# Optimization experiments

Hardware: AMD Instinct MI355X
Metric: run time of the kernel (lower is better)

## Reference

```python
import jax, jax.numpy as jnp
jax.config.update("jax_enable_x64", True)  # faithful to .double() matmul in original
import numpy as np

QMAX = 127.0  # int8 target: get_quant_min_max(torch.int8)[1]


def setup_inputs() -> dict:
    key = jax.random.key(0)
    k1, k2, k3, k4 = jax.random.split(key, 4)
    x = jax.random.normal(k1, (32768, 1024), dtype=jnp.float32)          # [tokens, cin]
    weight = jax.random.normal(k2, (1024, 1024), dtype=jnp.float32) * 0.02  # [cout, cin]
    bias = jax.random.normal(k3, (1024,), dtype=jnp.float32)             # [cout]
    # per-tensor activation scale from the (fake) observer; keep strictly positive
    act_scale = jax.random.uniform(k4, (1,), dtype=jnp.float32) * 0.05 + 0.01
    return {"x": x, "weight": weight, "bias": bias, "act_scale": act_scale}


def reference(x, weight, bias, act_scale):
    s = act_scale[0]  # per-tensor act scale; scale_input = 1/s
    # --- set_quantized_mode math ---
    w_scaled = weight * s                                        # fold act scale into weight (per-cin, per-tensor here)
    weight_scale = jnp.max(jnp.abs(w_scaled), axis=1) / QMAX     # [cout] per-output-channel scale
    qw = jnp.round(w_scaled / weight_scale[:, None])             # int8-valued weights (stored as float)
    # --- quantized forward ---
    xq = jnp.round(jnp.clip(x / s, -QMAX, QMAX))                 # fake-quant activations
    acc = jnp.matmul(xq.astype(jnp.float64), qw.astype(jnp.float64).T)  # double-precision GEMM
    y = acc.astype(jnp.float32) * weight_scale[None, :] + bias   # dequant rescale + bias
    return y
```

## Files before the change

### kernel.cpp

```cpp
#include <hip/hip_runtime.h>

typedef int i32x4 __attribute__((ext_vector_type(4)));

#define QMAXF 127.0f

__global__ __launch_bounds__(256) void quant_w_kernel(
    const float* __restrict__ w, const float* __restrict__ act_scale,
    signed char* __restrict__ qw, float* __restrict__ wscale)
{
    const int row = blockIdx.x;
    const int t   = threadIdx.x;
    const float s = act_scale[0];

    float4 v = *reinterpret_cast<const float4*>(w + (size_t)row * 1024 + t * 4);
    float a0 = v.x * s, a1 = v.y * s, a2 = v.z * s, a3 = v.w * s;
    float m = fmaxf(fmaxf(fabsf(a0), fabsf(a1)), fmaxf(fabsf(a2), fabsf(a3)));

    #pragma unroll
    for (int i = 1; i < 64; i <<= 1)
        m = fmaxf(m, __shfl_xor(m, i));

    __shared__ float wmax[4];
    if ((t & 63) == 0) wmax[t >> 6] = m;
    __syncthreads();
    m = fmaxf(fmaxf(wmax[0], wmax[1]), fmaxf(wmax[2], wmax[3]));

    const float wsc = m / QMAXF;

    int q0 = (int)rintf(a0 / wsc);
    int q1 = (int)rintf(a1 / wsc);
    int q2 = (int)rintf(a2 / wsc);
    int q3 = (int)rintf(a3 / wsc);
    int packed = (q0 & 255) | ((q1 & 255) << 8) | ((q2 & 255) << 16) | ((q3 & 255) << 24);
    reinterpret_cast<int*>(qw)[row * 256 + t] = packed;

    if (t == 0) wscale[row] = wsc;
}

__global__ __launch_bounds__(256) void quant_x_kernel(
    const float* __restrict__ x, const float* __restrict__ act_scale,
    signed char* __restrict__ xq)
{
    const float s = act_scale[0];
    const size_t i = ((size_t)blockIdx.x * 256 + threadIdx.x) * 4;
    float4 v = *reinterpret_cast<const float4*>(x + i);
    int q0 = (int)rintf(fminf(fmaxf(v.x / s, -QMAXF), QMAXF));
    int q1 = (int)rintf(fminf(fmaxf(v.y / s, -QMAXF), QMAXF));
    int q2 = (int)rintf(fminf(fmaxf(v.z / s, -QMAXF), QMAXF));
    int q3 = (int)rintf(fminf(fmaxf(v.w / s, -QMAXF), QMAXF));
    int packed = (q0 & 255) | ((q1 & 255) << 8) | ((q2 & 255) << 16) | ((q3 & 255) << 24);
    reinterpret_cast<int*>(xq)[i >> 2] = packed;
}

#define BM 256
#define BN 256
#define BKB 128
#define NTILES 8

#define BAR()   __builtin_amdgcn_s_barrier()
#define LGKM0() asm volatile("s_waitcnt lgkmcnt(0)" ::: "memory")

__global__ __launch_bounds__(512, 2) void gemm_i8_kernel(
    const signed char* __restrict__ xq, const signed char* __restrict__ qw,
    const float* __restrict__ wscale, const float* __restrict__ bias,
    float* __restrict__ out, int M)
{
    const int K = 1024, N = 1024;
    __shared__ __align__(16) signed char lds[2 * 2 * 2 * 16384];

    const int t    = threadIdx.x;
    const int lane = t & 63;
    const int w    = t >> 6;
    const int wr   = w >> 2;
    const int wc   = w & 3;
    const int lrow = lane & 15;
    const int ks   = lane >> 4;
    const int r8   = lane >> 3;
    const int sl   = lane & 7;

    const int nwg = gridDim.x;
    const int cpx = nwg >> 3;
    const int bid = blockIdx.x;
    const int swz = (bid & 7) * cpx + (bid >> 3);
    const int m0 = (swz >> 2) * BM;
    const int n0 = (swz & 3) * BN;

    i32x4 acc[8][4] = {};
    i32x4 Ar[4][2];
    i32x4 Br[2][2][2];

    auto STAGE = [&](int kt, int ab, int h) {
        const signed char* g = ab ? qw : xq;
        const int grow0 = (ab ? n0 : m0) + h * 128;
        signed char* lb = lds + (((kt & 1) * 2 + ab) * 2 + h) * 16384;
        #pragma unroll
        for (int j = 0; j < 2; ++j) {
            const int row = (j * 8 + w) * 8 + r8;
            const signed char* src =
                g + (size_t)(grow0 + row) * K + kt * BKB + ((sl ^ r8) << 4);
            __builtin_amdgcn_global_load_lds(
                (const __attribute__((address_space(1))) void*)src,
                (__attribute__((address_space(3))) void*)(lb + ((j * 8 + w) * 64 + lane) * 16),
                16, 0, 0);
        }
    };

    auto LDA = [&](int buf, int mh, i32x4 A[4][2]) {
        const signed char* base = lds + ((buf * 2 + 0) * 2 + wr) * 16384;
        #pragma unroll
        for (int mf = 0; mf < 4; ++mf) {
            const int row = mh * 64 + mf * 16 + lrow;
            #pragma unroll
            for (int kk = 0; kk < 2; ++kk) {
                const int slot = (kk * 4 + ks) ^ (lrow & 7);
                A[mf][kk] = *reinterpret_cast<const i32x4*>(base + row * 128 + slot * 16);
            }
        }
    };
    auto LDB = [&](int buf, int nh, i32x4 B[2][2]) {
        const signed char* base = lds + ((buf * 2 + 1) * 2 + (wc >> 1)) * 16384;
        #pragma unroll
        for (int nf = 0; nf < 2; ++nf) {
            const int row = (wc & 1) * 64 + nh * 32 + nf * 16 + lrow;
            #pragma unroll
            for (int kk = 0; kk < 2; ++kk) {
                const int slot = (kk * 4 + ks) ^ (lrow & 7);
                B[nf][kk] = *reinterpret_cast<const i32x4*>(base + row * 128 + slot * 16);
            }
        }
    };
    auto MM = [&](int mh, int nh, i32x4 A[4][2], i32x4 B[2][2]) {
        __builtin_amdgcn_s_setprio(1);
        #pragma unroll
        for (int mf = 0; mf < 4; ++mf)
            #pragma unroll
            for (int nf = 0; nf < 2; ++nf)
                #pragma unroll
                for (int kk = 0; kk < 2; ++kk)
                    acc[mh * 4 + mf][nh * 2 + nf] = __builtin_amdgcn_mfma_i32_16x16x64_i8(
                        A[mf][kk], B[nf][kk], acc[mh * 4 + mf][nh * 2 + nf], 0, 0, 0);
        __builtin_amdgcn_s_setprio(0);
    };

    STAGE(0, 1, 0); STAGE(0, 1, 1); STAGE(0, 0, 0); STAGE(0, 0, 1);
    STAGE(1, 1, 0); STAGE(1, 1, 1);
    asm volatile("s_waitcnt vmcnt(4)" ::: "memory");
    BAR();

    #pragma unroll
    for (int it = 0; it < NTILES / 2; ++it) {
        const int T = 2 * it;
        LDA(0, 0, Ar); LDB(0, 0, Br[0]);
        STAGE(T + 1, 0, 0);
        BAR(); LGKM0();
        MM(0, 0, Ar, Br[0]);
        BAR();
        LDB(0, 1, Br[1]);
        STAGE(T + 1, 0, 1);
        BAR(); LGKM0();
        MM(0, 1, Ar, Br[1]);
        BAR();
        LDA(0, 1, Ar);
        if (T + 2 < NTILES) STAGE(T + 2, 1, 0);
        BAR(); LGKM0();
        MM(1, 0, Ar, Br[0]);
        BAR();
        if (T + 2 < NTILES) STAGE(T + 2, 1, 1);
        MM(1, 1, Ar, Br[1]);
        if (T + 2 < NTILES) { asm volatile("s_waitcnt vmcnt(4)" ::: "memory"); }
        else                { asm volatile("s_waitcnt vmcnt(0)" ::: "memory"); }
        BAR();
        LDA(1, 0, Ar); LDB(1, 0, Br[0]);
        if (T + 2 < NTILES) STAGE(T + 2, 0, 0);
        BAR(); LGKM0();
        MM(0, 0, Ar, Br[0]);
        BAR();
        LDB(1, 1, Br[1]);
        if (T + 2 < NTILES) STAGE(T + 2, 0, 1);
        BAR(); LGKM0();
        MM(0, 1, Ar, Br[1]);
        BAR();
        LDA(1, 1, Ar);
        if (T + 3 < NTILES) STAGE(T + 3, 1, 0);
        BAR(); LGKM0();
        MM(1, 0, Ar, Br[0]);
        BAR();
        if (T + 3 < NTILES) STAGE(T + 3, 1, 1);
        MM(1, 1, Ar, Br[1]);
        if (T + 3 < NTILES) { asm volatile("s_waitcnt vmcnt(4)" ::: "memory"); }
        BAR();
    }

    float wsv[4], bv[4];
    int   gnc[4];
    #pragma unroll
    for (int nf = 0; nf < 4; ++nf) {
        const int gn = n0 + wc * 64 + nf * 16 + lrow;
        gnc[nf] = gn;
        wsv[nf] = wscale[gn];
        bv[nf]  = bias[gn];
    }
    #pragma unroll
    for (int mf = 0; mf < 8; ++mf) {
        #pragma unroll
        for (int r = 0; r < 4; ++r) {
            const int gm = m0 + wr * 128 + mf * 16 + ks * 4 + r;
            float* orow = out + (size_t)gm * N;
            #pragma unroll
            for (int nf = 0; nf < 4; ++nf)
                orow[gnc[nf]] = (float)acc[mf][nf][r] * wsv[nf] + bv[nf];
        }
    }
}

extern "C" void kernel_launch(void* const* d_in, const int* in_sizes, int n_in,
                              void* d_out, int out_size, void* d_ws, size_t ws_size,
                              hipStream_t stream)
{
    const float* x         = (const float*)d_in[0];
    const float* weight    = (const float*)d_in[1];
    const float* bias      = (const float*)d_in[2];
    const float* act_scale = (const float*)d_in[3];
    float* out             = (float*)d_out;

    const int K = 1024;
    const int N = 1024;
    const int M = in_sizes[0] / K;

    char* wsb = (char*)d_ws;
    signed char* qw  = (signed char*)wsb;
    float*       wsc = (float*)(wsb + (size_t)N * K);
    signed char* xq  = (signed char*)(wsb + (size_t)N * K + 4096);

    quant_w_kernel<<<N, 256, 0, stream>>>(weight, act_scale, qw, wsc);
    quant_x_kernel<<<(int)(((size_t)M * K) / 1024), 256, 0, stream>>>(x, act_scale, xq);

    const int grid = (M / BM) * (N / BN);
    gemm_i8_kernel<<<grid, 512, 0, stream>>>(xq, qw, wsc, bias, out, M);
}
```

Measured before the change: 86.35 us.

## Fuse activation quantization into int8 GEMM A-tile staging

Removes the separate activation-quantization kernel and its int8 intermediate buffer. The GEMM now loads fp32 x tiles into registers, quantizes them (multiplying by a reciprocal scale), and writes swizzled int8 into LDS. Only the weight tiles still go through direct global-to-LDS loads. The goal is to save one kernel launch plus the write and re-read of the quantized activations. In exchange, x is read as fp32 by each of the four column-tile blocks, which relies on L2 reuse. It also adds register pressure from the staged float4 buffers and drops the explicit vmcnt waits in favour of compiler-inserted waits.

Measured after the change: 216.3 us. +150.4%, slower.

```diff
diff --git a/kernel.cpp b/kernel.cpp
--- a/kernel.cpp
+++ b/kernel.cpp
@@ -3,6 +3,8 @@
 typedef int i32x4 __attribute__((ext_vector_type(4)));
 
 #define QMAXF 127.0f
+#define LGKM0() asm volatile("s_waitcnt lgkmcnt(0)" ::: "memory")
+#define BAR()   __builtin_amdgcn_s_barrier()
 
 __global__ __launch_bounds__(256) void quant_w_kernel(
     const float* __restrict__ w, const float* __restrict__ act_scale,
@@ -37,36 +39,16 @@
     if (t == 0) wscale[row] = wsc;
 }
 
-__global__ __launch_bounds__(256) void quant_x_kernel(
-    const float* __restrict__ x, const float* __restrict__ act_scale,
-    signed char* __restrict__ xq)
-{
-    const float s = act_scale[0];
-    const size_t i = ((size_t)blockIdx.x * 256 + threadIdx.x) * 4;
-    float4 v = *reinterpret_cast<const float4*>(x + i);
-    int q0 = (int)rintf(fminf(fmaxf(v.x / s, -QMAXF), QMAXF));
-    int q1 = (int)rintf(fminf(fmaxf(v.y / s, -QMAXF), QMAXF));
-    int q2 = (int)rintf(fminf(fmaxf(v.z / s, -QMAXF), QMAXF));
-    int q3 = (int)rintf(fminf(fmaxf(v.w / s, -QMAXF), QMAXF));
-    int packed = (q0 & 255) | ((q1 & 255) << 8) | ((q2 & 255) << 16) | ((q3 & 255) << 24);
-    reinterpret_cast<int*>(xq)[i >> 2] = packed;
-}
-
-#define BM 256
-#define BN 256
-#define BKB 128
 #define NTILES 8
 
-#define BAR()   __builtin_amdgcn_s_barrier()
-#define LGKM0() asm volatile("s_waitcnt lgkmcnt(0)" ::: "memory")
-
-__global__ __launch_bounds__(512, 2) void gemm_i8_kernel(
-    const signed char* __restrict__ xq, const signed char* __restrict__ qw,
-    const float* __restrict__ wscale, const float* __restrict__ bias,
-    float* __restrict__ out, int M)
+__global__ __launch_bounds__(512, 2) void gemm_fused_kernel(
+    const float* __restrict__ x, const signed char* __restrict__ qw,
+    const float* __restrict__ act_scale, const float* __restrict__ wscale,
+    const float* __restrict__ bias, float* __restrict__ out, int M)
 {
     const int K = 1024, N = 1024;
-    __shared__ __align__(16) signed char lds[2 * 2 * 2 * 16384];
+    __shared__ __align__(16) signed char As[4][16384];
+    __shared__ __align__(16) signed char Bs[4][16384];
 
     const int t    = threadIdx.x;
     const int lane = t & 63;
@@ -77,48 +59,72 @@
     const int ks   = lane >> 4;
     const int r8   = lane >> 3;
     const int sl   = lane & 7;
+    const int ar   = t >> 2;
+    const int ac2  = t & 3;
 
     const int nwg = gridDim.x;
     const int cpx = nwg >> 3;
     const int bid = blockIdx.x;
     const int swz = (bid & 7) * cpx + (bid >> 3);
-    const int m0 = (swz >> 2) * BM;
-    const int n0 = (swz & 3) * BN;
+    const int m0 = (swz >> 2) * 256;
+    const int n0 = (swz & 3) * 256;
+
+    const float rinv = 1.0f / act_scale[0];
 
     i32x4 acc[8][4] = {};
     i32x4 Ar[4][2];
     i32x4 Br[2][2][2];
-
-    auto STAGE = [&](int kt, int ab, int h) {
-        const signed char* g = ab ? qw : xq;
-        const int grow0 = (ab ? n0 : m0) + h * 128;
-        signed char* lb = lds + (((kt & 1) * 2 + ab) * 2 + h) * 16384;
+    float4 X0[8], X1[8];
+
+    auto STAGE_B = [&](int kt, int h) {
+        signed char* lb = &Bs[(kt & 1) * 2 + h][0];
         #pragma unroll
         for (int j = 0; j < 2; ++j) {
-            const int row = (j * 8 + w) * 8 + r8;
+            const int rowh = (j * 8 + w) * 8 + r8;
             const signed char* src =
-                g + (size_t)(grow0 + row) * K + kt * BKB + ((sl ^ r8) << 4);
+                qw + (size_t)(n0 + h * 128 + rowh) * K + kt * 128 + ((sl ^ r8) << 4);
             __builtin_amdgcn_global_load_lds(
                 (const __attribute__((address_space(1))) void*)src,
                 (__attribute__((address_space(3))) void*)(lb + ((j * 8 + w) * 64 + lane) * 16),
                 16, 0, 0);
         }
     };
-
-    auto LDA = [&](int buf, int mh, i32x4 A[4][2]) {
-        const signed char* base = lds + ((buf * 2 + 0) * 2 + wr) * 16384;
+    auto XLD = [&](int kt, int h, float4 (&X)[8]) {
+        const float* p = x + (size_t)(m0 + h * 128 + ar) * K + kt * 128 + ac2 * 32;
+        #pragma unroll
+        for (int j = 0; j < 8; ++j) X[j] = *reinterpret_cast<const float4*>(p + j * 4);
+    };
+    auto AQW = [&](int kt, int h, const float4 (&X)[8]) {
+        int pk[8];
+        #pragma unroll
+        for (int c = 0; c < 8; ++c) {
+            int q0 = (int)rintf(fminf(fmaxf(X[c].x * rinv, -QMAXF), QMAXF));
+            int q1 = (int)rintf(fminf(fmaxf(X[c].y * rinv, -QMAXF), QMAXF));
+            int q2 = (int)rintf(fminf(fmaxf(X[c].z * rinv, -QMAXF), QMAXF));
+            int q3 = (int)rintf(fminf(fmaxf(X[c].w * rinv, -QMAXF), QMAXF));
+            pk[c] = (q0 & 255) | ((q1 & 255) << 8) | ((q2 & 255) << 16) | ((q3 & 255) << 24);
+        }
+        signed char* base = &As[(kt & 1) * 2 + h][0];
+        const int g0 = 2 * ac2, g1 = 2 * ac2 + 1;
+        *reinterpret_cast<i32x4*>(base + ar * 128 + ((g0 ^ (ar & 7)) << 4)) =
+            i32x4{pk[0], pk[1], pk[2], pk[3]};
+        *reinterpret_cast<i32x4*>(base + ar * 128 + ((g1 ^ (ar & 7)) << 4)) =
+            i32x4{pk[4], pk[5], pk[6], pk[7]};
+    };
+    auto LDA = [&](int buf, int mh) {
+        const signed char* base = &As[buf * 2 + wr][0];
         #pragma unroll
         for (int mf = 0; mf < 4; ++mf) {
             const int row = mh * 64 + mf * 16 + lrow;
             #pragma unroll
             for (int kk = 0; kk < 2; ++kk) {
                 const int slot = (kk * 4 + ks) ^ (lrow & 7);
-                A[mf][kk] = *reinterpret_cast<const i32x4*>(base + row * 128 + slot * 16);
+                Ar[mf][kk] = *reinterpret_cast<const i32x4*>(base + row * 128 + slot * 16);
             }
         }
     };
-    auto LDB = [&](int buf, int nh, i32x4 B[2][2]) {
-        const signed char* base = lds + ((buf * 2 + 1) * 2 + (wc >> 1)) * 16384;
+    auto LDB = [&](int buf, int nh, i32x4 (&B)[2][2]) {
+        const signed char* base = &Bs[buf * 2 + (wc >> 1)][0];
         #pragma unroll
         for (int nf = 0; nf < 2; ++nf) {
             const int row = (wc & 1) * 64 + nh * 32 + nf * 16 + lrow;
@@ -129,7 +135,7 @@
             }
         }
     };
-    auto MM = [&](int mh, int nh, i32x4 A[4][2], i32x4 B[2][2]) {
+    auto MM = [&](int mh, int nh, i32x4 (&B)[2][2]) {
         __builtin_amdgcn_s_setprio(1);
         #pragma unroll
         for (int mf = 0; mf < 4; ++mf)
@@ -138,57 +144,59 @@
                 #pragma unroll
                 for (int kk = 0; kk < 2; ++kk)
                     acc[mh * 4 + mf][nh * 2 + nf] = __builtin_amdgcn_mfma_i32_16x16x64_i8(
-                        A[mf][kk], B[nf][kk], acc[mh * 4 + mf][nh * 2 + nf], 0, 0, 0);
+                        Ar[mf][kk], B[nf][kk], acc[mh * 4 + mf][nh * 2 + nf], 0, 0, 0);
         __builtin_amdgcn_s_setprio(0);
     };
 
-    STAGE(0, 1, 0); STAGE(0, 1, 1); STAGE(0, 0, 0); STAGE(0, 0, 1);
-    STAGE(1, 1, 0); STAGE(1, 1, 1);
-    asm volatile("s_waitcnt vmcnt(4)" ::: "memory");
-    BAR();
+    STAGE_B(0, 0); STAGE_B(0, 1);
+    XLD(0, 0, X0); XLD(0, 1, X1);
+    AQW(0, 0, X0); AQW(0, 1, X1);
+    STAGE_B(1, 0); STAGE_B(1, 1);
+    LGKM0(); BAR();
 
     #pragma unroll
     for (int it = 0; it < NTILES / 2; ++it) {
         const int T = 2 * it;
-        LDA(0, 0, Ar); LDB(0, 0, Br[0]);
-        STAGE(T + 1, 0, 0);
-        BAR(); LGKM0();
-        MM(0, 0, Ar, Br[0]);
+        LDA(0, 0); LDB(0, 0, Br[0]);
+        XLD(T + 1, 0, X0);
+        BAR(); LGKM0();
+        MM(0, 0, Br[0]);
         BAR();
         LDB(0, 1, Br[1]);
-        STAGE(T + 1, 0, 1);
-        BAR(); LGKM0();
-        MM(0, 1, Ar, Br[1]);
-        BAR();
-        LDA(0, 1, Ar);
-        if (T + 2 < NTILES) STAGE(T + 2, 1, 0);
-        BAR(); LGKM0();
-        MM(1, 0, Ar, Br[0]);
-        BAR();
-        if (T + 2 < NTILES) STAGE(T + 2, 1, 1);
-        MM(1, 1, Ar, Br[1]);
-        if (T + 2 < NTILES) { asm volatile("s_waitcnt vmcnt(4)" ::: "memory"); }
-        else                { asm volatile("s_waitcnt vmcnt(0)" ::: "memory"); }
-        BAR();
-        LDA(1, 0, Ar); LDB(1, 0, Br[0]);
-        if (T + 2 < NTILES) STAGE(T + 2, 0, 0);
-        BAR(); LGKM0();
-        MM(0, 0, Ar, Br[0]);
+        XLD(T + 1, 1, X1);
+        BAR(); LGKM0();
+        MM(0, 1, Br[1]);
+        BAR();
+        LDA(0, 1);
+        if (T + 2 < NTILES) STAGE_B(T + 2, 0);
+        AQW(T + 1, 0, X0);
+        LGKM0(); BAR();
+        MM(1, 0, Br[0]);
+        BAR();
+        if (T + 2 < NTILES) STAGE_B(T + 2, 1);
+        AQW(T + 1, 1, X1);
+        MM(1, 1, Br[1]);
+        LGKM0(); BAR();
+        LDA(1, 0); LDB(1, 0, Br[0]);
+        if (T + 2 < NTILES) XLD(T + 2, 0, X0);
+        BAR(); LGKM0();
+        MM(0, 0, Br[0]);
         BAR();
         LDB(1, 1, Br[1]);
-        if (T + 2 < NTILES) STAGE(T + 2, 0, 1);
-        BAR(); LGKM0();
-        MM(0, 1, Ar, Br[1]);
-        BAR();
-        LDA(1, 1, Ar);
-        if (T + 3 < NTILES) STAGE(T + 3, 1, 0);
-        BAR(); LGKM0();
-        MM(1, 0, Ar, Br[0]);
-        BAR();
-        if (T + 3 < NTILES) STAGE(T + 3, 1, 1);
-        MM(1, 1, Ar, Br[1]);
-        if (T + 3 < NTILES) { asm volatile("s_waitcnt vmcnt(4)" ::: "memory"); }
-        BAR();
+        if (T + 2 < NTILES) XLD(T + 2, 1, X1);
+        BAR(); LGKM0();
+        MM(0, 1, Br[1]);
+        BAR();
+        LDA(1, 1);
+        if (T + 3 < NTILES) STAGE_B(T + 3, 0);
+        if (T + 2 < NTILES) AQW(T + 2, 0, X0);
+        LGKM0(); BAR();
+        MM(1, 0, Br[0]);
+        BAR();
+        if (T + 3 < NTILES) STAGE_B(T + 3, 1);
+        if (T + 2 < NTILES) AQW(T + 2, 1, X1);
+        MM(1, 1, Br[1]);
+        LGKM0(); BAR();
     }
 
     float wsv[4], bv[4];
@@ -230,11 +238,9 @@
     char* wsb = (char*)d_ws;
     signed char* qw  = (signed char*)wsb;
     float*       wsc = (float*)(wsb + (size_t)N * K);
-    signed char* xq  = (signed char*)(wsb + (size_t)N * K + 4096);
 
     quant_w_kernel<<<N, 256, 0, stream>>>(weight, act_scale, qw, wsc);
-    quant_x_kernel<<<(int)(((size_t)M * K) / 1024), 256, 0, stream>>>(x, act_scale, xq);
-
-    const int grid = (M / BM) * (N / BN);
-    gemm_i8_kernel<<<grid, 512, 0, stream>>>(xq, qw, wsc, bias, out, M);
+
+    const int grid = (M / 256) * (N / 256);
+    gemm_fused_kernel<<<grid, 512, 0, stream>>>(x, qw, act_scale, wsc, bias, out, M);
 }
```
